# Kernel tuning notes

Measured on AMD Instinct MI355X. Metric: run time of the kernel, lower is better.

The kernel has to match this reference:

```python
import jax, jax.numpy as jnp
import numpy as np

N_SPK = 2048   # number of speakers
U = 32         # utterances per speaker (half enrollment, half test)
D = 256        # embedding dim
EPS = 1e-8     # F.cosine_similarity eps (norm clamp)


def setup_inputs() -> dict:
    key = jax.random.key(0)
    k1, = jax.random.split(key, 1)
    embeddings = jax.random.normal(k1, (N_SPK * U, D), dtype=jnp.float32)
    labels = jnp.repeat(jnp.arange(N_SPK, dtype=jnp.int64), U)
    alpha = jnp.float32(10.0)
    beta = jnp.float32(-5.0)
    return {"embeddings": embeddings, "labels": labels, "alpha": alpha, "beta": beta}


def _ge2e_loss(embeddings, labels_np, alpha, beta):
    # labels_np: host numpy int labels (constant). Balanced: each speaker has U utts.
    n_spk = int(labels_np.max()) + 1
    u = labels_np.shape[0] // n_spk
    order = np.argsort(labels_np, kind="stable")  # group by speaker, preserve order
    emb = embeddings[order].reshape(n_spk, u, -1)           # [N, U, D]
    half = u // 2
    enroll, test = emb[:, :half], emb[:, half:]             # [N, U/2, D]
    cent = enroll.mean(axis=1)                              # [N, D]
    tn = test / jnp.maximum(jnp.linalg.norm(test, axis=-1, keepdims=True), EPS)
    cn = cent / jnp.maximum(jnp.linalg.norm(cent, axis=-1, keepdims=True), EPS)
    # cosine sim of every test utt (speaker m, utt t) vs every centroid n
    sims = alpha * jnp.einsum("mtd,nd->mtn", tn, cn) + beta  # [N, U/2, N]
    e = jnp.exp(sims)
    total = e.sum(axis=(0, 1))                               # [N] sum over all test utts per centroid
    idx = jnp.arange(n_spk)
    pos_sum = e[idx, :, idx].sum(axis=1)                     # [N] own-speaker test utts
    neg_sum = total - pos_sum                                # sum over other speakers' test utts
    loss = jnp.mean(jnp.log(neg_sum) - jnp.log(pos_sum))
    return loss


def reference(embeddings, labels, alpha, beta):
    labels_np = np.asarray(labels)
    return _ge2e_loss(embeddings, labels_np, alpha, beta)
```

## Files before the change

### kernel.cpp

```cpp
#include <hip/hip_runtime.h>
#include <hip/hip_bf16.h>
#include <stdint.h>

#define N_SPK 2048
#define UU 32
#define DD 256
#define HALF_U 16
#define M_ROWS (N_SPK * HALF_U)

#define BM 256
#define BN 256
#define BK 64

typedef __attribute__((ext_vector_type(8))) short short8;
typedef __attribute__((ext_vector_type(4))) float f32x4;

typedef const __attribute__((address_space(1))) void ga_void;
typedef __attribute__((address_space(3))) void ls_void;

__device__ __forceinline__ void gld16(const void* g, void* l) {
    __builtin_amdgcn_global_load_lds((ga_void*)(uintptr_t)g,
                                     (ls_void*)(uintptr_t)l, 16, 0, 0);
}

__device__ __forceinline__ unsigned short f2bf(float x) {
    union { float f; unsigned u; } c; c.f = x;
    unsigned r = c.u + 0x7fffu + ((c.u >> 16) & 1u);
    return (unsigned short)(r >> 16);
}

#define WAITVM(n) do { \
    asm volatile("s_waitcnt vmcnt(" #n ")" ::: "memory"); \
    __builtin_amdgcn_sched_barrier(0); \
} while (0)

#define WAITLGKM0 do { \
    asm volatile("s_waitcnt lgkmcnt(0)" ::: "memory"); \
    __builtin_amdgcn_sched_barrier(0); \
} while (0)

__global__ __launch_bounds__(256) void prep_kernel(const float* __restrict__ emb,
                                                   unsigned short* __restrict__ tn,
                                                   unsigned short* __restrict__ cn,
                                                   float* __restrict__ zbuf)
{
    if (blockIdx.x == 0) {
        #pragma unroll
        for (int i = 0; i < 16; ++i) zbuf[threadIdx.x + 256 * i] = 0.0f;
    }

    const int w = threadIdx.x >> 6;
    const int l = threadIdx.x & 63;
    const int task = blockIdx.x * 4 + w;

    float4 v;
    if (task < M_ROWS) {
        const int m = task >> 4;
        const int t = task & 15;
        const size_t grow = (size_t)m * UU + HALF_U + t;
        v = *(const float4*)(emb + grow * DD + 4 * l);
    } else {
        const int n = task - M_ROWS;
        float ax = 0.f, ay = 0.f, az = 0.f, aw = 0.f;
        const float* base = emb + (size_t)n * UU * DD + 4 * l;
        #pragma unroll
        for (int j = 0; j < HALF_U; ++j) {
            float4 e = *(const float4*)(base + j * DD);
            ax += e.x; ay += e.y; az += e.z; aw += e.w;
        }
        const float inv = 1.0f / 16.0f;
        v = make_float4(ax * inv, ay * inv, az * inv, aw * inv);
    }
    float ss = v.x * v.x + v.y * v.y + v.z * v.z + v.w * v.w;
    #pragma unroll
    for (int d = 1; d < 64; d <<= 1) ss += __shfl_xor(ss, d);
    const float sc = 1.0f / fmaxf(sqrtf(ss), 1e-8f);

    ushort4 o;
    o.x = f2bf(v.x * sc); o.y = f2bf(v.y * sc);
    o.z = f2bf(v.z * sc); o.w = f2bf(v.w * sc);
    unsigned short* dst = (task < M_ROWS)
        ? (tn + (size_t)task * DD + 4 * l)
        : (cn + (size_t)(task - M_ROWS) * DD + 4 * l);
    *(ushort4*)dst = o;
}

__global__ __launch_bounds__(512, 2) void gemm_kernel(const unsigned short* __restrict__ tnb,
                                                      const unsigned short* __restrict__ cnb,
                                                      const float* __restrict__ alphaP,
                                                      const float* __restrict__ betaP,
                                                      float* __restrict__ total,
                                                      float* __restrict__ pos)
{
    __shared__ __align__(16) char S[4][32768];

    const int tid = threadIdx.x;
    const int l = tid & 63;
    const int w = tid >> 6;
    const int wr = w >> 2, wc = w & 3;
    const int r16 = l & 15, hi = l >> 4;

    const float alpha = *alphaP;
    const float beta  = *betaP;

    const int bid = blockIdx.x;
    const int tile = (bid & 7) * 128 + (bid >> 3);
    const int bm = tile >> 3;
    const int bn = tile & 7;

    const char* gA = (const char*)tnb + (size_t)bm * BM * 512;
    const char* gB = (const char*)cnb + (size_t)bn * BN * 512;

    auto stage_unit = [&](int kt, int u) {
        const int h = u >> 1;
        const int mat = u & 1;
        char* slot = S[(2 * kt + h) & 3] + mat * 16384;
        const char* g = mat ? gB : gA;
        #pragma unroll
        for (int i = 0; i < 2; ++i) {
            const int off = i * 8192 + tid * 16;
            const int row = off >> 7;
            const int sc  = ((off >> 4) & 7) ^ (row & 7);
            const int goff = (h * 128 + row) * 512 + kt * 128 + sc * 16;
            gld16(g + goff, slot + off);
        }
    };

    f32x4 acc[8][4] = {};

    #pragma unroll
    for (int u = 0; u < 4; ++u) stage_unit(0, u);
    #pragma unroll
    for (int u = 0; u < 4; ++u) stage_unit(1, u);
    WAITVM(8);
    __builtin_amdgcn_s_barrier();

    #pragma unroll
    for (int kt = 0; kt < 4; ++kt) {
        const char* As = S[(2 * kt + wr) & 3];
        const char* Bs = S[(2 * kt + (wc >> 1)) & 3] + 16384;
        short8 b[4][2];
        #pragma unroll
        for (int p = 0; p < 4; ++p) {
            short8 a[2][2];
            if (p == 0) {
                #pragma unroll
                for (int ni = 0; ni < 4; ++ni)
                    #pragma unroll
                    for (int kk = 0; kk < 2; ++kk) {
                        const int row = wc * 64 + ni * 16 + r16;
                        const int c16 = (kk * 4 + hi) ^ (row & 7);
                        b[ni][kk] = *(const short8*)(Bs + (row & 127) * 128 + c16 * 16);
                    }
            }
            #pragma unroll
            for (int m2 = 0; m2 < 2; ++m2)
                #pragma unroll
                for (int kk = 0; kk < 2; ++kk) {
                    const int mi = p * 2 + m2;
                    const int lrow = mi * 16 + r16;
                    const int c16 = (kk * 4 + hi) ^ (lrow & 7);
                    a[m2][kk] = *(const short8*)(As + lrow * 128 + c16 * 16);
                }
            if (kt == 1 || kt == 2) {
                if (p == 0) { stage_unit(kt + 1, 0); stage_unit(kt + 1, 1); }
                if (p == 1) { stage_unit(kt + 1, 2); stage_unit(kt + 1, 3); }
            }
            __builtin_amdgcn_s_barrier();
            WAITLGKM0;
            __builtin_amdgcn_s_setprio(1);
            #pragma unroll
            for (int kk = 0; kk < 2; ++kk)
                #pragma unroll
                for (int m2 = 0; m2 < 2; ++m2)
                    #pragma unroll
                    for (int ni = 0; ni < 4; ++ni)
                        acc[p * 2 + m2][ni] = __builtin_amdgcn_mfma_f32_16x16x32_bf16(
                            a[m2][kk], b[ni][kk], acc[p * 2 + m2][ni], 0, 0, 0);
            __builtin_amdgcn_s_setprio(0);
            __builtin_amdgcn_s_barrier();
        }
        if (kt < 3) {
            WAITVM(0);
            __builtin_amdgcn_s_barrier();
        }
    }

    float* colsum = (float*)S;
    __syncthreads();
    if (tid < BN) colsum[tid] = 0.0f;
    __syncthreads();

    #pragma unroll
    for (int ni = 0; ni < 4; ++ni) {
        const int colg = bn * BN + wc * 64 + ni * 16 + r16;
        float csum = 0.f;
        #pragma unroll
        for (int mi = 0; mi < 8; ++mi) {
            const int rowbase = bm * BM + wr * 128 + mi * 16 + hi * 4;
            #pragma unroll
            for (int r = 0; r < 4; ++r) {
                const float e = __expf(alpha * acc[mi][ni][r] + beta);
                csum += e;
                if (((rowbase + r) >> 4) == colg)
                    atomicAdd(pos + colg, e);
            }
        }
        csum += __shfl_xor(csum, 16);
        csum += __shfl_xor(csum, 32);
        if (hi == 0) atomicAdd(&colsum[wc * 64 + ni * 16 + r16], csum);
    }
    __syncthreads();
    if (tid < BN) atomicAdd(total + bn * BN + tid, colsum[tid]);
}

__global__ __launch_bounds__(256) void finalize_kernel(const float* __restrict__ total,
                                                       const float* __restrict__ pos,
                                                       float* __restrict__ out)
{
    const int tid = threadIdx.x;
    float s = 0.f;
    for (int i = tid; i < N_SPK; i += 256) {
        const float p = pos[i];
        const float t = total[i];
        s += logf(t - p) - logf(p);
    }
    #pragma unroll
    for (int d = 1; d < 64; d <<= 1) s += __shfl_xor(s, d);
    __shared__ float wsum[4];
    if ((tid & 63) == 0) wsum[tid >> 6] = s;
    __syncthreads();
    if (tid == 0) out[0] = (wsum[0] + wsum[1] + wsum[2] + wsum[3]) * (1.0f / (float)N_SPK);
}

extern "C" void kernel_launch(void* const* d_in, const int* in_sizes, int n_in,
                              void* d_out, int out_size, void* d_ws, size_t ws_size,
                              hipStream_t stream)
{
    const float* emb    = (const float*)d_in[0];
    const float* alphaP = (const float*)d_in[2];
    const float* betaP  = (const float*)d_in[3];
    float* out = (float*)d_out;

    char* ws = (char*)d_ws;
    unsigned short* tn = (unsigned short*)ws;
    unsigned short* cn = (unsigned short*)(ws + 16777216);
    float* total       = (float*)(ws + 16777216 + 1048576);
    float* pos         = total + N_SPK;

    hipLaunchKernelGGL(prep_kernel, dim3((M_ROWS + N_SPK) / 4), dim3(256), 0, stream,
                       emb, tn, cn, total );
    hipLaunchKernelGGL(gemm_kernel, dim3(M_ROWS / BM * (N_SPK / BN)), dim3(512), 0, stream,
                       tn, cn, alphaP, betaP, total, pos);
    hipLaunchKernelGGL(finalize_kernel, dim3(1), dim3(256), 0, stream,
                       total, pos, out);
}
```

Before: 157.8 us.

## Make GEMM persistent over four column tiles with continuous K pipeline

Each block now handles one row tile across four column tiles, 256 blocks in total instead of 1024. The K-loop runs for 16 steps and streams across tile boundaries, so loads for the next tile overlap the epilogue of the current one and the per-tile prologue is gone. The epilogue now runs in-loop every four steps, reuses a dedicated shared colsum, and only does pos atomics on diagonal tiles. The risks are lower occupancy and less parallelism with 256 blocks on a 256-CU device, plus extra barriers in the epilogue.

```diff
diff --git a/kernel.cpp b/kernel.cpp
--- a/kernel.cpp
+++ b/kernel.cpp
@@ -93,6 +93,7 @@
                                                       float* __restrict__ pos)
 {
     __shared__ __align__(16) char S[4][32768];
+    __shared__ float csum[BN];
 
     const int tid = threadIdx.x;
     const int l = tid & 63;
@@ -103,42 +104,39 @@
     const float alpha = *alphaP;
     const float beta  = *betaP;
 
-    const int bid = blockIdx.x;
-    const int tile = (bid & 7) * 128 + (bid >> 3);
-    const int bm = tile >> 3;
-    const int bn = tile & 7;
+    const int c = blockIdx.x;
+    const int xcd = c & 7, slot = c >> 3;
+    const int bm = xcd * 16 + (slot >> 1);
+    const int bn0 = (slot & 1) * 4;
 
     const char* gA = (const char*)tnb + (size_t)bm * BM * 512;
-    const char* gB = (const char*)cnb + (size_t)bn * BN * 512;
-
-    auto stage_unit = [&](int kt, int u) {
-        const int h = u >> 1;
-        const int mat = u & 1;
-        char* slot = S[(2 * kt + h) & 3] + mat * 16384;
-        const char* g = mat ? gB : gA;
+
+    auto stage_half = [&](int jj, int h) {
+        const int kt = jj & 3;
+        const int bn = bn0 + (jj >> 2);
+        char* slotp = S[(2 * jj + h) & 3];
+        const char* gB = (const char*)cnb + (size_t)bn * BN * 512;
         #pragma unroll
         for (int i = 0; i < 2; ++i) {
             const int off = i * 8192 + tid * 16;
             const int row = off >> 7;
             const int sc  = ((off >> 4) & 7) ^ (row & 7);
             const int goff = (h * 128 + row) * 512 + kt * 128 + sc * 16;
-            gld16(g + goff, slot + off);
+            gld16(gA + goff, slotp + off);
+            gld16(gB + goff, slotp + 16384 + off);
         }
     };
 
     f32x4 acc[8][4] = {};
 
-    #pragma unroll
-    for (int u = 0; u < 4; ++u) stage_unit(0, u);
-    #pragma unroll
-    for (int u = 0; u < 4; ++u) stage_unit(1, u);
+    stage_half(0, 0); stage_half(0, 1);
+    stage_half(1, 0); stage_half(1, 1);
     WAITVM(8);
     __builtin_amdgcn_s_barrier();
 
-    #pragma unroll
-    for (int kt = 0; kt < 4; ++kt) {
-        const char* As = S[(2 * kt + wr) & 3];
-        const char* Bs = S[(2 * kt + (wc >> 1)) & 3] + 16384;
+    for (int j = 0; j < 16; ++j) {
+        const char* As = S[(2 * j + wr) & 3];
+        const char* Bs = S[(2 * j + (wc >> 1)) & 3] + 16384;
         short8 b[4][2];
         #pragma unroll
         for (int p = 0; p < 4; ++p) {
@@ -162,9 +160,9 @@
                     const int c16 = (kk * 4 + hi) ^ (lrow & 7);
                     a[m2][kk] = *(const short8*)(As + lrow * 128 + c16 * 16);
                 }
-            if (kt == 1 || kt == 2) {
-                if (p == 0) { stage_unit(kt + 1, 0); stage_unit(kt + 1, 1); }
-                if (p == 1) { stage_unit(kt + 1, 2); stage_unit(kt + 1, 3); }
+            if (j < 15) {
+                if (p == 0) stage_half(j + 1, 0);
+                if (p == 1) stage_half(j + 1, 1);
             }
             __builtin_amdgcn_s_barrier();
             WAITLGKM0;
@@ -180,38 +178,42 @@
             __builtin_amdgcn_s_setprio(0);
             __builtin_amdgcn_s_barrier();
         }
-        if (kt < 3) {
+
+        if ((j & 3) == 3) {
+            const int bn = bn0 + (j >> 2);
+            const bool diag = ((bm >> 4) == bn);
+            if (tid < BN) csum[tid] = 0.0f;
+            __builtin_amdgcn_s_barrier();
+            #pragma unroll
+            for (int ni = 0; ni < 4; ++ni) {
+                const int colg = bn * BN + wc * 64 + ni * 16 + r16;
+                float cs = 0.f;
+                #pragma unroll
+                for (int mi = 0; mi < 8; ++mi) {
+                    const int rowbase = bm * BM + wr * 128 + mi * 16 + hi * 4;
+                    #pragma unroll
+                    for (int r = 0; r < 4; ++r) {
+                        const float e = __expf(alpha * acc[mi][ni][r] + beta);
+                        cs += e;
+                        if (diag && ((rowbase + r) >> 4) == colg)
+                            atomicAdd(pos + colg, e);
+                    }
+                    acc[mi][ni] = (f32x4){0.f, 0.f, 0.f, 0.f};
+                }
+                cs += __shfl_xor(cs, 16);
+                cs += __shfl_xor(cs, 32);
+                if (hi == 0) atomicAdd(&csum[wc * 64 + ni * 16 + r16], cs);
+            }
+            __builtin_amdgcn_s_barrier();
+            if (tid < BN) atomicAdd(total + bn * BN + tid, csum[tid]);
+            __builtin_amdgcn_s_barrier();
+        }
+
+        if (j < 15) {
             WAITVM(0);
             __builtin_amdgcn_s_barrier();
         }
     }
-
-    float* colsum = (float*)S;
-    __syncthreads();
-    if (tid < BN) colsum[tid] = 0.0f;
-    __syncthreads();
-
-    #pragma unroll
-    for (int ni = 0; ni < 4; ++ni) {
-        const int colg = bn * BN + wc * 64 + ni * 16 + r16;
-        float csum = 0.f;
-        #pragma unroll
-        for (int mi = 0; mi < 8; ++mi) {
-            const int rowbase = bm * BM + wr * 128 + mi * 16 + hi * 4;
-            #pragma unroll
-            for (int r = 0; r < 4; ++r) {
-                const float e = __expf(alpha * acc[mi][ni][r] + beta);
-                csum += e;
-                if (((rowbase + r) >> 4) == colg)
-                    atomicAdd(pos + colg, e);
-            }
-        }
-        csum += __shfl_xor(csum, 16);
-        csum += __shfl_xor(csum, 32);
-        if (hi == 0) atomicAdd(&colsum[wc * 64 + ni * 16 + r16], csum);
-    }
-    __syncthreads();
-    if (tid < BN) atomicAdd(total + bn * BN + tid, colsum[tid]);
 }
 
 __global__ __launch_bounds__(256) void finalize_kernel(const float* __restrict__ total,
@@ -250,7 +252,7 @@
 
     hipLaunchKernelGGL(prep_kernel, dim3((M_ROWS + N_SPK) / 4), dim3(256), 0, stream,
                        emb, tn, cn, total );
-    hipLaunchKernelGGL(gemm_kernel, dim3(M_ROWS / BM * (N_SPK / BN)), dim3(512), 0, stream,
+    hipLaunchKernelGGL(gemm_kernel, dim3(256), dim3(512), 0, stream,
                        tn, cn, alphaP, betaP, total, pos);
     hipLaunchKernelGGL(finalize_kernel, dim3(1), dim3(256), 0, stream,
                        total, pos, out);
```

Measured after the change: 155.9 us. No clear change (-1.2%).
